# Kernel tuning notes

Hardware: AMD Instinct MI355X
Metric: run time of the kernel (lower is better)

## Reference

```python
import jax, jax.numpy as jnp
import numpy as np

B, N, C = 32, 320, 768
H = 12
LT, LS = 64, 256
HD = C // H
MLP_H = 4 * C
EPS = 1e-5


def _ln(x, g, b):
    m = jnp.mean(x, axis=-1, keepdims=True)
    v = jnp.var(x, axis=-1, keepdims=True)
    return (x - m) * jax.lax.rsqrt(v + EPS) * g + b


def setup_inputs() -> dict:
    key = jax.random.key(0)
    ks = jax.random.split(key, 16)
    s = 0.02
    inp = {
        'x': jax.random.normal(ks[0], (B, N, C), jnp.float32),
        'global_index_template': jax.random.randint(ks[1], (B, LT), 0, LT),
        'global_index_search': jax.random.randint(ks[2], (B, LS), 0, LS),
        'g1': jnp.ones((C,), jnp.float32), 'b1': jnp.zeros((C,), jnp.float32),
        'Wqkv': jax.random.normal(ks[3], (C, 3 * C), jnp.float32) * s,
        'Wproj': jax.random.normal(ks[4], (C, C), jnp.float32) * s,
        'bproj': jnp.zeros((C,), jnp.float32),
        'g2': jnp.ones((C,), jnp.float32), 'b2': jnp.zeros((C,), jnp.float32),
        'W1': jax.random.normal(ks[5], (C, MLP_H), jnp.float32) * s,
        'bm1': jnp.zeros((MLP_H,), jnp.float32),
        'W2': jax.random.normal(ks[6], (MLP_H, C), jnp.float32) * s,
        'bm2': jnp.zeros((C,), jnp.float32),
        'Wg': jax.random.normal(ks[7], (C, C), jnp.float32) * s,
        'bg': jnp.zeros((C,), jnp.float32),
        'g3': jnp.ones((C,), jnp.float32), 'b3': jnp.zeros((C,), jnp.float32),
    }
    return inp


def reference(x, global_index_template, global_index_search, g1, b1, Wqkv, Wproj, bproj,
              g2, b2, W1, bm1, W2, bm2, Wg, bg, g3, b3):
    scale = HD ** (-0.5)
    # --- Attention ---
    xn = _ln(x, g1, b1)
    qkv = (xn @ Wqkv).reshape(B, N, 3, H, HD)
    q, k, v = qkv[:, :, 0], qkv[:, :, 1], qkv[:, :, 2]  # [B,N,H,HD]
    logits = jnp.einsum('bnhd,bmhd->bhnm', q, k) * scale
    attn = jax.nn.softmax(logits, axis=-1)  # [B,H,N,N]
    ctx = jnp.einsum('bhnm,bmhd->bnhd', attn, v).reshape(B, N, C)
    x = x + (ctx @ Wproj + bproj)
    # --- MLP ---
    h = jax.nn.gelu(_ln(x, g2, b2) @ W1 + bm1, approximate=False)
    x = x + (h @ W2 + bm2)
    # --- Block-adjacency from attention (avg pooling) ---
    w_ts = jnp.sum(attn[:, :, :LT, LT:], axis=1) / H  # [B,LT,LS]
    w_ts = jax.nn.softmax(w_ts, axis=2)
    adj = jnp.zeros((B, N, N), x.dtype)
    adj = adj.at[:, :LT, LT:].set(w_ts)
    adj = adj.at[:, LT:, :LT].set(jnp.swapaxes(w_ts, 1, 2))
    # --- GCN layer ---
    support = x @ Wg + bg
    x = jnp.einsum('bnm,bmc->bnc', adj, support)
    x = x + _ln(x, g3, b3)
    return x
```

## Files before the change

### kernel.cpp

```cpp
#include <hip/hip_runtime.h>
#include <stdint.h>

#define NB 32
#define NSEQ 320
#define CDIM 768
#define NH 12
#define HD 64
#define MLPH 3072
#define MROWS (NB*NSEQ)

typedef __attribute__((ext_vector_type(8))) short v8s;
typedef __attribute__((ext_vector_type(4))) float v4f;

__device__ __forceinline__ unsigned short f2b(float f){
  unsigned int u = __float_as_uint(f);
  u += 0x7fffu + ((u >> 16) & 1u);
  return (unsigned short)(u >> 16);
}
__device__ __forceinline__ float b2f(unsigned short h){
  return __uint_as_float(((unsigned int)h) << 16);
}
__device__ __forceinline__ void glds16(const unsigned short* g, unsigned short* l){
  __builtin_amdgcn_global_load_lds(
      (const __attribute__((address_space(1))) void*)g,
      (__attribute__((address_space(3))) void*)l, 16, 0, 0);
}

__global__ __launch_bounds__(256)
void castT(const float* __restrict__ W, unsigned short* __restrict__ Wt, int K, int N){
  __shared__ float tile[32][33];
  const int k0 = blockIdx.x * 32, n0 = blockIdx.y * 32;
  const int tx = threadIdx.x & 31, ty = threadIdx.x >> 5;
  #pragma unroll
  for (int i = 0; i < 32; i += 8)
    tile[ty + i][tx] = W[(size_t)(k0 + ty + i) * N + n0 + tx];
  __syncthreads();
  #pragma unroll
  for (int i = 0; i < 32; i += 8)
    Wt[(size_t)(n0 + ty + i) * K + k0 + tx] = f2b(tile[tx][ty + i]);
}

__global__ __launch_bounds__(192)
void ln_to_bf16(const float* __restrict__ x, const float* __restrict__ g,
                const float* __restrict__ be, unsigned short* __restrict__ out){
  const int row = blockIdx.x;
  const int t = threadIdx.x, w = t >> 6, l = t & 63;
  const float4 v = *(const float4*)(x + (size_t)row * CDIM + t * 4);
  float s  = v.x + v.y + v.z + v.w;
  float s2 = v.x*v.x + v.y*v.y + v.z*v.z + v.w*v.w;
  __shared__ float r1[3], r2[3];
  #pragma unroll
  for (int d = 1; d < 64; d <<= 1){ s += __shfl_xor(s, d, 64); s2 += __shfl_xor(s2, d, 64); }
  if (l == 0){ r1[w] = s; r2[w] = s2; }
  __syncthreads();
  const float S = r1[0] + r1[1] + r1[2];
  const float S2 = r2[0] + r2[1] + r2[2];
  const float mean = S * (1.0f / CDIM);
  const float var  = S2 * (1.0f / CDIM) - mean * mean;
  const float rs = rsqrtf(var + 1e-5f);
  const float4 gg = *(const float4*)(g + t * 4);
  const float4 bb = *(const float4*)(be + t * 4);
  ushort4 o;
  o.x = f2b((v.x - mean) * rs * gg.x + bb.x);
  o.y = f2b((v.y - mean) * rs * gg.y + bb.y);
  o.z = f2b((v.z - mean) * rs * gg.z + bb.z);
  o.w = f2b((v.w - mean) * rs * gg.w + bb.w);
  *(ushort4*)(out + (size_t)row * CDIM + t * 4) = o;
}

template<bool BIAS, bool RES, bool GELU, bool WB, bool WF>
__global__ __launch_bounds__(256, 2)
void gemm_bt(const unsigned short* __restrict__ A, const unsigned short* __restrict__ Bt,
             int M, int N, int K,
             const float* __restrict__ bias, const float* __restrict__ res,
             unsigned short* __restrict__ outb, float* __restrict__ outf){
  __shared__ __align__(16) unsigned short As[128 * 32];
  __shared__ __align__(16) unsigned short Bs[128 * 32];
  const int t = threadIdx.x;
  const int w = t >> 6, l = t & 63;
  const int bm = blockIdx.x, bn = blockIdx.y;
  const int wr = w >> 1, wc = w & 1;
  v4f acc[4][4] = {};

  const int srow = (w << 5) + (l >> 2);
  const int sseg = (l & 3) * 8;
  const unsigned short* Ag = A + (size_t)(bm * 128 + srow) * K + sseg;
  const unsigned short* Bg = Bt + (size_t)(bn * 128 + srow) * K + sseg;
  unsigned short* Al = As + (w * 32) * 32;
  unsigned short* Bl = Bs + (w * 32) * 32;

  const int ksteps = K >> 5;
  for (int ks = 0; ks < ksteps; ++ks){
    const int k0 = ks << 5;
    if (ks) __syncthreads();
    glds16(Ag + k0, Al);
    glds16(Ag + (size_t)16 * K + k0, Al + 16 * 32);
    glds16(Bg + k0, Bl);
    glds16(Bg + (size_t)16 * K + k0, Bl + 16 * 32);
    __syncthreads();
    const int kk = (l >> 4) << 3;
    v8s af[4], bfr[4];
    #pragma unroll
    for (int mi = 0; mi < 4; ++mi)
      af[mi] = *(const v8s*)&As[(wr * 64 + mi * 16 + (l & 15)) * 32 + kk];
    #pragma unroll
    for (int ni = 0; ni < 4; ++ni)
      bfr[ni] = *(const v8s*)&Bs[(wc * 64 + ni * 16 + (l & 15)) * 32 + kk];
    #pragma unroll
    for (int mi = 0; mi < 4; ++mi)
      #pragma unroll
      for (int ni = 0; ni < 4; ++ni)
        acc[mi][ni] = __builtin_amdgcn_mfma_f32_16x16x32_bf16(af[mi], bfr[ni], acc[mi][ni], 0, 0, 0);
  }

  const int r0 = bm * 128 + wr * 64 + ((l >> 4) << 2);
  const int c0 = bn * 128 + wc * 64 + (l & 15);
  #pragma unroll
  for (int mi = 0; mi < 4; ++mi){
    #pragma unroll
    for (int rr = 0; rr < 4; ++rr){
      const int row = r0 + mi * 16 + rr;
      #pragma unroll
      for (int ni = 0; ni < 4; ++ni){
        const int col = c0 + ni * 16;
        float c = acc[mi][ni][rr];
        if (BIAS) c += bias[col];
        if (RES)  c += res[(size_t)row * N + col];
        if (GELU) c = 0.5f * c * (1.0f + erff(c * 0.70710678118f));
        if (WB) outb[(size_t)row * N + col] = f2b(c);
        if (WF) outf[(size_t)row * N + col] = c;
      }
    }
  }
}

__global__ __launch_bounds__(256, 2)
void attn_kernel(const unsigned short* __restrict__ qkv,
                 unsigned short* __restrict__ ctx,
                 float* __restrict__ wparts){
  __shared__ __align__(16) unsigned short Qs[64 * 72];
  __shared__ __align__(16) unsigned short KV[64 * 72];
  __shared__ __align__(16) unsigned short Ps[64 * 328];
  const int t = threadIdx.x;
  const int w = t >> 6, l = t & 63;
  const int bid = blockIdx.x;
  const int qt = bid % 5;
  const int h  = (bid / 5) % NH;
  const int b  = bid / (5 * NH);
  const size_t base = (size_t)b * NSEQ * 2304 + h * 64;

  {
    const int r = t >> 3, seg = t & 7;
    #pragma unroll
    for (int i = 0; i < 2; ++i){
      const int r2 = r + 32 * i;
      const unsigned short* src = qkv + base + (size_t)(qt * 64 + r2) * 2304 + seg * 8;
      *(uint4*)&Qs[r2 * 72 + seg * 8] = *(const uint4*)src;
    }
  }
  __syncthreads();
  const int qr = 16 * w + (l & 15);
  const v8s aq0 = *(const v8s*)&Qs[qr * 72 + ((l >> 4) << 3)];
  const v8s aq1 = *(const v8s*)&Qs[qr * 72 + 32 + ((l >> 4) << 3)];

  v4f sacc[20] = {};
  for (int kt = 0; kt < 5; ++kt){
    __syncthreads();
    {
      const int r = t >> 3, seg = t & 7;
      #pragma unroll
      for (int i = 0; i < 2; ++i){
        const int r2 = r + 32 * i;
        const unsigned short* src = qkv + base + 768 + (size_t)(kt * 64 + r2) * 2304 + seg * 8;
        *(uint4*)&KV[r2 * 72 + seg * 8] = *(const uint4*)src;
      }
    }
    __syncthreads();
    #pragma unroll
    for (int f = 0; f < 4; ++f){
      const int kr = 16 * f + (l & 15);
      const v8s b0 = *(const v8s*)&KV[kr * 72 + ((l >> 4) << 3)];
      const v8s b1 = *(const v8s*)&KV[kr * 72 + 32 + ((l >> 4) << 3)];
      sacc[kt * 4 + f] = __builtin_amdgcn_mfma_f32_16x16x32_bf16(aq0, b0, sacc[kt * 4 + f], 0, 0, 0);
      sacc[kt * 4 + f] = __builtin_amdgcn_mfma_f32_16x16x32_bf16(aq1, b1, sacc[kt * 4 + f], 0, 0, 0);
    }
  }

  const float scale = 0.125f;
  #pragma unroll
  for (int r = 0; r < 4; ++r){
    float m = -1e30f;
    #pragma unroll
    for (int f = 0; f < 20; ++f) m = fmaxf(m, sacc[f][r]);
    #pragma unroll
    for (int d = 1; d < 16; d <<= 1) m = fmaxf(m, __shfl_xor(m, d, 64));
    const float Ms = m * scale;
    float sum = 0.f;
    #pragma unroll
    for (int f = 0; f < 20; ++f){ float p = expf(sacc[f][r] * scale - Ms); sacc[f][r] = p; sum += p; }
    #pragma unroll
    for (int d = 1; d < 16; d <<= 1) sum += __shfl_xor(sum, d, 64);
    const float inv = 1.0f / sum;
    const int rowq = 16 * w + ((l >> 4) << 2) + r;
    #pragma unroll
    for (int f = 0; f < 20; ++f)
      Ps[rowq * 328 + f * 16 + (l & 15)] = f2b(sacc[f][r] * inv);
    if (qt == 0){
      #pragma unroll
      for (int f = 4; f < 20; ++f)
        wparts[(((size_t)b * NH + h) * 64 + rowq) * 256 + (f - 4) * 16 + (l & 15)] = sacc[f][r] * inv;
    }
  }

  v4f cacc[4] = {};
  for (int kt = 0; kt < 5; ++kt){
    __syncthreads();
    {
      const int m = t & 31, d0 = (t >> 5) * 8;
      #pragma unroll
      for (int i = 0; i < 2; ++i){
        const int m2 = m + 32 * i;
        const unsigned short* src = qkv + base + 1536 + (size_t)(kt * 64 + m2) * 2304 + d0;
        uint4 dv = *(const uint4*)src;
        const unsigned short* e = (const unsigned short*)&dv;
        #pragma unroll
        for (int jj = 0; jj < 8; ++jj) KV[(d0 + jj) * 72 + m2] = e[jj];
      }
    }
    __syncthreads();
    const int pr = 16 * w + (l & 15);
    const v8s pa0 = *(const v8s*)&Ps[pr * 328 + kt * 64 + ((l >> 4) << 3)];
    const v8s pa1 = *(const v8s*)&Ps[pr * 328 + kt * 64 + 32 + ((l >> 4) << 3)];
    #pragma unroll
    for (int f = 0; f < 4; ++f){
      const int vc = 16 * f + (l & 15);
      const v8s bv0 = *(const v8s*)&KV[vc * 72 + ((l >> 4) << 3)];
      const v8s bv1 = *(const v8s*)&KV[vc * 72 + 32 + ((l >> 4) << 3)];
      cacc[f] = __builtin_amdgcn_mfma_f32_16x16x32_bf16(pa0, bv0, cacc[f], 0, 0, 0);
      cacc[f] = __builtin_amdgcn_mfma_f32_16x16x32_bf16(pa1, bv1, cacc[f], 0, 0, 0);
    }
  }
  #pragma unroll
  for (int f = 0; f < 4; ++f)
    #pragma unroll
    for (int rr = 0; rr < 4; ++rr){
      const int rowq = 16 * w + ((l >> 4) << 2) + rr;
      const int col = 16 * f + (l & 15);
      ctx[(size_t)(b * NSEQ + qt * 64 + rowq) * CDIM + h * 64 + col] = f2b(cacc[f][rr]);
    }
}

__global__ __launch_bounds__(256)
void wts_softmax(const float* __restrict__ wparts, float* __restrict__ wts){
  const int row = blockIdx.x;
  const int b = row >> 6, n = row & 63;
  const int j = threadIdx.x;
  const int w = j >> 6, l = j & 63;
  float s = 0.f;
  #pragma unroll
  for (int hh = 0; hh < NH; ++hh)
    s += wparts[(((size_t)b * NH + hh) * 64 + n) * 256 + j];
  s *= (1.0f / NH);
  __shared__ float red[8];
  float m = s;
  #pragma unroll
  for (int d = 1; d < 64; d <<= 1) m = fmaxf(m, __shfl_xor(m, d, 64));
  if (l == 0) red[w] = m;
  __syncthreads();
  m = fmaxf(fmaxf(red[0], red[1]), fmaxf(red[2], red[3]));
  const float e = expf(s - m);
  float sm = e;
  #pragma unroll
  for (int d = 1; d < 64; d <<= 1) sm += __shfl_xor(sm, d, 64);
  if (l == 0) red[4 + w] = sm;
  __syncthreads();
  const float tot = red[4] + red[5] + red[6] + red[7];
  wts[(size_t)row * 256 + j] = e / tot;
}

__global__ __launch_bounds__(192)
void graph_final(const float* __restrict__ wts, const unsigned short* __restrict__ sup,
                 const float* __restrict__ g3, const float* __restrict__ b3,
                 float* __restrict__ out){
  const int bid = blockIdx.x;
  const int n = bid % NSEQ;
  const int b = bid / NSEQ;
  const int t = threadIdx.x, w = t >> 6, l = t & 63;
  __shared__ float wl[256];
  __shared__ float r1[3], r2[3];
  int kk, srow0;
  if (n < 64){
    kk = 256; srow0 = b * NSEQ + 64;
    for (int j = t; j < 256; j += 192) wl[j] = wts[(size_t)(b * 64 + n) * 256 + j];
  } else {
    kk = 64; srow0 = b * NSEQ;
    const int jj = n - 64;
    for (int i = t; i < 64; i += 192) wl[i] = wts[(size_t)(b * 64 + i) * 256 + jj];
  }
  __syncthreads();
  float a0 = 0, a1 = 0, a2 = 0, a3 = 0;
  for (int j = 0; j < kk; ++j){
    const float wv = wl[j];
    const uint2 sv = *(const uint2*)&sup[(size_t)(srow0 + j) * CDIM + t * 4];
    a0 += wv * b2f((unsigned short)(sv.x & 0xffff));
    a1 += wv * b2f((unsigned short)(sv.x >> 16));
    a2 += wv * b2f((unsigned short)(sv.y & 0xffff));
    a3 += wv * b2f((unsigned short)(sv.y >> 16));
  }
  float s = a0 + a1 + a2 + a3;
  float s2 = a0*a0 + a1*a1 + a2*a2 + a3*a3;
  #pragma unroll
  for (int d = 1; d < 64; d <<= 1){ s += __shfl_xor(s, d, 64); s2 += __shfl_xor(s2, d, 64); }
  if (l == 0){ r1[w] = s; r2[w] = s2; }
  __syncthreads();
  const float S = r1[0] + r1[1] + r1[2], S2 = r2[0] + r2[1] + r2[2];
  const float mean = S * (1.0f / CDIM);
  const float var = S2 * (1.0f / CDIM) - mean * mean;
  const float rs = rsqrtf(var + 1e-5f);
  const float4 gg = *(const float4*)&g3[t * 4];
  const float4 bb = *(const float4*)&b3[t * 4];
  float4 o;
  o.x = a0 + (a0 - mean) * rs * gg.x + bb.x;
  o.y = a1 + (a1 - mean) * rs * gg.y + bb.y;
  o.z = a2 + (a2 - mean) * rs * gg.z + bb.z;
  o.w = a3 + (a3 - mean) * rs * gg.w + bb.w;
  *(float4*)&out[(size_t)bid * CDIM + t * 4] = o;
}

extern "C" void kernel_launch(void* const* d_in, const int* in_sizes, int n_in,
                              void* d_out, int out_size, void* d_ws, size_t ws_size,
                              hipStream_t stream){
  (void)in_sizes; (void)n_in; (void)out_size; (void)ws_size;
  const float* x    = (const float*)d_in[0];
  const float* g1   = (const float*)d_in[3];
  const float* b1   = (const float*)d_in[4];
  const float* Wqkv = (const float*)d_in[5];
  const float* Wproj= (const float*)d_in[6];
  const float* bproj= (const float*)d_in[7];
  const float* g2   = (const float*)d_in[8];
  const float* b2   = (const float*)d_in[9];
  const float* W1   = (const float*)d_in[10];
  const float* bm1  = (const float*)d_in[11];
  const float* W2   = (const float*)d_in[12];
  const float* bm2  = (const float*)d_in[13];
  const float* Wg   = (const float*)d_in[14];
  const float* bg   = (const float*)d_in[15];
  const float* g3   = (const float*)d_in[16];
  const float* b3   = (const float*)d_in[17];
  float* out = (float*)d_out;
  char* ws = (char*)d_ws;

  unsigned short* wqkvT = (unsigned short*)(ws + 0);
  unsigned short* wprojT= (unsigned short*)(ws + 3538944);
  unsigned short* w1T   = (unsigned short*)(ws + 4718592);
  unsigned short* w2T   = (unsigned short*)(ws + 9437184);
  unsigned short* wgT   = (unsigned short*)(ws + 14155776);
  unsigned short* xn1   = (unsigned short*)(ws + 15335424);
  unsigned short* qkvb  = (unsigned short*)(ws + 31064064);
  unsigned short* hb    = (unsigned short*)(ws + 15335424);
  unsigned short* ctxb  = (unsigned short*)(ws + 78249984);
  unsigned short* x2b   = (unsigned short*)(ws + 78249984);
  unsigned short* xn2   = (unsigned short*)(ws + 93978624);
  unsigned short* supb  = (unsigned short*)(ws + 93978624);
  float*          x1    = (float*)(ws + 109707264);
  float*          wparts= (float*)(ws + 109707264);
  float*          wts   = (float*)(ws + 141164544);

  castT<<<dim3(CDIM/32, 2304/32), 256, 0, stream>>>(Wqkv, wqkvT, CDIM, 2304);
  castT<<<dim3(CDIM/32, CDIM/32), 256, 0, stream>>>(Wproj, wprojT, CDIM, CDIM);
  castT<<<dim3(CDIM/32, MLPH/32), 256, 0, stream>>>(W1, w1T, CDIM, MLPH);
  castT<<<dim3(MLPH/32, CDIM/32), 256, 0, stream>>>(W2, w2T, MLPH, CDIM);
  castT<<<dim3(CDIM/32, CDIM/32), 256, 0, stream>>>(Wg, wgT, CDIM, CDIM);

  ln_to_bf16<<<MROWS, 192, 0, stream>>>(x, g1, b1, xn1);

  gemm_bt<false,false,false,true,false><<<dim3(80, 18), 256, 0, stream>>>(
      xn1, wqkvT, MROWS, 2304, CDIM, nullptr, nullptr, qkvb, nullptr);

  attn_kernel<<<NB * NH * 5, 256, 0, stream>>>(qkvb, ctxb, wparts);

  wts_softmax<<<NB * 64, 256, 0, stream>>>(wparts, wts);

  gemm_bt<true,true,false,false,true><<<dim3(80, 6), 256, 0, stream>>>(
      ctxb, wprojT, MROWS, CDIM, CDIM, bproj, x, nullptr, x1);

  ln_to_bf16<<<MROWS, 192, 0, stream>>>(x1, g2, b2, xn2);

  gemm_bt<true,false,true,true,false><<<dim3(80, 24), 256, 0, stream>>>(
      xn2, w1T, MROWS, MLPH, CDIM, bm1, nullptr, hb, nullptr);

  gemm_bt<true,true,false,true,false><<<dim3(80, 6), 256, 0, stream>>>(
      hb, w2T, MROWS, CDIM, MLPH, bm2, x1, x2b, nullptr);

  gemm_bt<true,false,false,true,false><<<dim3(80, 6), 256, 0, stream>>>(
      x2b, wgT, MROWS, CDIM, CDIM, bg, nullptr, supb, nullptr);

  graph_final<<<MROWS, 192, 0, stream>>>(wts, supb, g3, b3, out);
}
```

Baseline: 564.8 us.

## Replace scalar graph aggregation with transposed-support MFMA GEMMs and separate LayerNorm

The per-row scalar loop that multiplied the adjacency weights by the support matrix is replaced by bf16 MFMA GEMMs. The support matrix is first transposed per batch, and the adjacency weights are stored in bf16 in both orientations. Two GEMM launches cover the template rows (K=256) and the search rows (K=64), write fp32 results, and a separate kernel then applies the residual LayerNorm. This trades the scalar FMA loop with poor reuse for tensor-core work, at the cost of an extra transpose, an extra fp32 round trip, bf16 rounding of the weights, and two more launches.

```diff
diff --git a/kernel.cpp b/kernel.cpp
--- a/kernel.cpp
+++ b/kernel.cpp
@@ -251,7 +251,9 @@
 }
 
 __global__ __launch_bounds__(256)
-void wts_softmax(const float* __restrict__ wparts, float* __restrict__ wts){
+void wts_softmax(const float* __restrict__ wparts,
+                 unsigned short* __restrict__ wtsb,
+                 unsigned short* __restrict__ wtsbT){
   const int row = blockIdx.x;
   const int b = row >> 6, n = row & 63;
   const int j = threadIdx.x;
@@ -275,56 +277,128 @@
   if (l == 0) red[4 + w] = sm;
   __syncthreads();
   const float tot = red[4] + red[5] + red[6] + red[7];
-  wts[(size_t)row * 256 + j] = e / tot;
+  const unsigned short p = f2b(e / tot);
+  wtsb [((size_t)b * 64 + n) * 256 + j] = p;
+  wtsbT[((size_t)b * 256 + j) * 64 + n] = p;
+}
+
+__global__ __launch_bounds__(256)
+void transT(const unsigned short* __restrict__ in, unsigned short* __restrict__ out){
+  __shared__ unsigned short tile[64][65];
+  const int c0 = blockIdx.x * 64, n0 = blockIdx.y * 64, b = blockIdx.z;
+  const int tx = threadIdx.x & 31, ty = threadIdx.x >> 5;
+  const unsigned short* ib = in + (size_t)b * NSEQ * CDIM;
+  unsigned short* ob = out + (size_t)b * CDIM * NSEQ;
+  #pragma unroll
+  for (int i = 0; i < 64; i += 8){
+    const unsigned int v = *(const unsigned int*)&ib[(size_t)(n0 + ty + i) * CDIM + c0 + tx * 2];
+    tile[tx * 2][ty + i]     = (unsigned short)(v & 0xffff);
+    tile[tx * 2 + 1][ty + i] = (unsigned short)(v >> 16);
+  }
+  __syncthreads();
+  #pragma unroll
+  for (int i = 0; i < 64; i += 8){
+    const int c = ty + i;
+    const unsigned int v = (unsigned int)tile[c][tx * 2] | ((unsigned int)tile[c][tx * 2 + 1] << 16);
+    *(unsigned int*)&ob[(size_t)(c0 + c) * NSEQ + n0 + tx * 2] = v;
+  }
+}
+
+template<int KC, int SH2>
+__global__ __launch_bounds__(256, 2)
+void graph_gemm(const unsigned short* __restrict__ A, int KTOT,
+                const unsigned short* __restrict__ supT, int koff,
+                float* __restrict__ y, int rowoff){
+  __shared__ __align__(16) unsigned short As[64 * KC];
+  __shared__ __align__(16) unsigned short Bs[128 * KC];
+  const int t = threadIdx.x, w = t >> 6, l = t & 63;
+  const int mt = blockIdx.x, ct = blockIdx.y, b = blockIdx.z;
+  const char* Ab = (const char*)(A + (size_t)b * 16384 + (size_t)mt * 64 * KTOT);
+  const char* Bb = (const char*)(supT + (size_t)b * CDIM * NSEQ);
+  v4f acc[4][2] = {};
+
+  const int nch = KTOT / KC;
+  for (int ch = 0; ch < nch; ++ch){
+    if (ch) __syncthreads();
+    const int kbase = (koff + ch * KC) * 2;
+    #pragma unroll
+    for (int i = 0; i < KC / 32; ++i){
+      const int gi = w * (KC / 32) + i;
+      const int X = gi * 1024 + l * 16;
+      const int c = X >> SH2;
+      const int k2 = (X & (KC * 2 - 1)) ^ ((c & 7) << 4);
+      glds16((const unsigned short*)(Ab + (size_t)c * (KTOT * 2) + ch * KC * 2 + k2),
+             As + (gi * 512));
+    }
+    #pragma unroll
+    for (int i = 0; i < KC / 16; ++i){
+      const int gi = w * (KC / 16) + i;
+      const int X = gi * 1024 + l * 16;
+      const int c = X >> SH2;
+      const int k2 = (X & (KC * 2 - 1)) ^ ((c & 7) << 4);
+      glds16((const unsigned short*)(Bb + (size_t)(ct * 128 + c) * (NSEQ * 2) + kbase + k2),
+             Bs + (gi * 512));
+    }
+    __syncthreads();
+    #pragma unroll
+    for (int ks = 0; ks < KC / 32; ++ks){
+      const int kbyte = ks * 64 + ((l >> 4) << 4);
+      v8s af[4], bf2[2];
+      #pragma unroll
+      for (int mi = 0; mi < 4; ++mi){
+        const int r = mi * 16 + (l & 15);
+        af[mi] = *(const v8s*)((const char*)As + (r << SH2) + (kbyte ^ ((r & 7) << 4)));
+      }
+      #pragma unroll
+      for (int ni = 0; ni < 2; ++ni){
+        const int rb = w * 32 + ni * 16 + (l & 15);
+        bf2[ni] = *(const v8s*)((const char*)Bs + (rb << SH2) + (kbyte ^ ((rb & 7) << 4)));
+      }
+      #pragma unroll
+      for (int mi = 0; mi < 4; ++mi)
+        #pragma unroll
+        for (int ni = 0; ni < 2; ++ni)
+          acc[mi][ni] = __builtin_amdgcn_mfma_f32_16x16x32_bf16(af[mi], bf2[ni], acc[mi][ni], 0, 0, 0);
+    }
+  }
+
+  const int r0 = rowoff + mt * 64 + ((l >> 4) << 2);
+  const int c0 = ct * 128 + w * 32 + (l & 15);
+  #pragma unroll
+  for (int mi = 0; mi < 4; ++mi)
+    #pragma unroll
+    for (int ni = 0; ni < 2; ++ni)
+      #pragma unroll
+      for (int rr = 0; rr < 4; ++rr)
+        y[((size_t)b * NSEQ + r0 + mi * 16 + rr) * CDIM + c0 + ni * 16] = acc[mi][ni][rr];
 }
 
 __global__ __launch_bounds__(192)
-void graph_final(const float* __restrict__ wts, const unsigned short* __restrict__ sup,
-                 const float* __restrict__ g3, const float* __restrict__ b3,
-                 float* __restrict__ out){
-  const int bid = blockIdx.x;
-  const int n = bid % NSEQ;
-  const int b = bid / NSEQ;
+void ln_final(const float* __restrict__ y, const float* __restrict__ g3,
+              const float* __restrict__ b3, float* __restrict__ out){
+  const int row = blockIdx.x;
   const int t = threadIdx.x, w = t >> 6, l = t & 63;
-  __shared__ float wl[256];
+  const float4 v = *(const float4*)(y + (size_t)row * CDIM + t * 4);
+  float s  = v.x + v.y + v.z + v.w;
+  float s2 = v.x*v.x + v.y*v.y + v.z*v.z + v.w*v.w;
   __shared__ float r1[3], r2[3];
-  int kk, srow0;
-  if (n < 64){
-    kk = 256; srow0 = b * NSEQ + 64;
-    for (int j = t; j < 256; j += 192) wl[j] = wts[(size_t)(b * 64 + n) * 256 + j];
-  } else {
-    kk = 64; srow0 = b * NSEQ;
-    const int jj = n - 64;
-    for (int i = t; i < 64; i += 192) wl[i] = wts[(size_t)(b * 64 + i) * 256 + jj];
-  }
-  __syncthreads();
-  float a0 = 0, a1 = 0, a2 = 0, a3 = 0;
-  for (int j = 0; j < kk; ++j){
-    const float wv = wl[j];
-    const uint2 sv = *(const uint2*)&sup[(size_t)(srow0 + j) * CDIM + t * 4];
-    a0 += wv * b2f((unsigned short)(sv.x & 0xffff));
-    a1 += wv * b2f((unsigned short)(sv.x >> 16));
-    a2 += wv * b2f((unsigned short)(sv.y & 0xffff));
-    a3 += wv * b2f((unsigned short)(sv.y >> 16));
-  }
-  float s = a0 + a1 + a2 + a3;
-  float s2 = a0*a0 + a1*a1 + a2*a2 + a3*a3;
   #pragma unroll
   for (int d = 1; d < 64; d <<= 1){ s += __shfl_xor(s, d, 64); s2 += __shfl_xor(s2, d, 64); }
   if (l == 0){ r1[w] = s; r2[w] = s2; }
   __syncthreads();
-  const float S = r1[0] + r1[1] + r1[2], S2 = r2[0] + r2[1] + r2[2];
+  const float S = r1[0] + r1[1] + r1[2];
+  const float S2 = r2[0] + r2[1] + r2[2];
   const float mean = S * (1.0f / CDIM);
-  const float var = S2 * (1.0f / CDIM) - mean * mean;
+  const float var  = S2 * (1.0f / CDIM) - mean * mean;
   const float rs = rsqrtf(var + 1e-5f);
-  const float4 gg = *(const float4*)&g3[t * 4];
-  const float4 bb = *(const float4*)&b3[t * 4];
+  const float4 gg = *(const float4*)(g3 + t * 4);
+  const float4 bb = *(const float4*)(b3 + t * 4);
   float4 o;
-  o.x = a0 + (a0 - mean) * rs * gg.x + bb.x;
-  o.y = a1 + (a1 - mean) * rs * gg.y + bb.y;
-  o.z = a2 + (a2 - mean) * rs * gg.z + bb.z;
-  o.w = a3 + (a3 - mean) * rs * gg.w + bb.w;
-  *(float4*)&out[(size_t)bid * CDIM + t * 4] = o;
+  o.x = v.x + (v.x - mean) * rs * gg.x + bb.x;
+  o.y = v.y + (v.y - mean) * rs * gg.y + bb.y;
+  o.z = v.z + (v.z - mean) * rs * gg.z + bb.z;
+  o.w = v.w + (v.w - mean) * rs * gg.w + bb.w;
+  *(float4*)(out + (size_t)row * CDIM + t * 4) = o;
 }
 
 extern "C" void kernel_launch(void* const* d_in, const int* in_sizes, int n_in,
@@ -358,13 +432,16 @@
   unsigned short* xn1   = (unsigned short*)(ws + 15335424);
   unsigned short* qkvb  = (unsigned short*)(ws + 31064064);
   unsigned short* hb    = (unsigned short*)(ws + 15335424);
+  unsigned short* supT  = (unsigned short*)(ws + 15335424);
   unsigned short* ctxb  = (unsigned short*)(ws + 78249984);
   unsigned short* x2b   = (unsigned short*)(ws + 78249984);
   unsigned short* xn2   = (unsigned short*)(ws + 93978624);
   unsigned short* supb  = (unsigned short*)(ws + 93978624);
   float*          x1    = (float*)(ws + 109707264);
   float*          wparts= (float*)(ws + 109707264);
-  float*          wts   = (float*)(ws + 141164544);
+  float*          yb    = (float*)(ws + 109707264);
+  unsigned short* wtsb  = (unsigned short*)(ws + 141164544);
+  unsigned short* wtsbT = (unsigned short*)(ws + 142213120);
 
   castT<<<dim3(CDIM/32, 2304/32), 256, 0, stream>>>(Wqkv, wqkvT, CDIM, 2304);
   castT<<<dim3(CDIM/32, CDIM/32), 256, 0, stream>>>(Wproj, wprojT, CDIM, CDIM);
@@ -379,7 +456,7 @@
 
   attn_kernel<<<NB * NH * 5, 256, 0, stream>>>(qkvb, ctxb, wparts);
 
-  wts_softmax<<<NB * 64, 256, 0, stream>>>(wparts, wts);
+  wts_softmax<<<NB * 64, 256, 0, stream>>>(wparts, wtsb, wtsbT);
 
   gemm_bt<true,true,false,false,true><<<dim3(80, 6), 256, 0, stream>>>(
       ctxb, wprojT, MROWS, CDIM, CDIM, bproj, x, nullptr, x1);
@@ -395,5 +472,10 @@
   gemm_bt<true,false,false,true,false><<<dim3(80, 6), 256, 0, stream>>>(
       x2b, wgT, MROWS, CDIM, CDIM, bg, nullptr, supb, nullptr);
 
-  graph_final<<<MROWS, 192, 0, stream>>>(wts, supb, g3, b3, out);
-}
+  transT<<<dim3(CDIM/64, NSEQ/64, NB), 256, 0, stream>>>(supb, supT);
+
+  graph_gemm<128, 8><<<dim3(1, 6, NB), 256, 0, stream>>>(wtsb, 256, supT, 64, yb, 0);
+  graph_gemm<64, 7><<<dim3(4, 6, NB), 256, 0, stream>>>(wtsbT, 64, supT, 0, yb, 64);
+
+  ln_final<<<MROWS, 192, 0, stream>>>(yb, g3, b3, out);
+}
```

New measurement: 502.0 us. 1.13x faster.
